# Kernel tuning notes

Measured on AMD Instinct MI355X. Metric: run time of the kernel, lower is better.

## Reference

```python
import jax, jax.numpy as jnp
import numpy as np

N_OUT = 1024

def setup_inputs() -> dict:
    key = jax.random.key(0)
    k1, k2, k3 = jax.random.split(key, 3)
    L, B, n_in = 2048, 16, 1024
    inp = {
        "input": jax.random.normal(k1, (L, B, n_in), dtype=jnp.float32),
        "c_init": jnp.zeros((B, N_OUT), dtype=jnp.float32),
        "weight": jax.random.normal(k2, (n_in, 2 * N_OUT), dtype=jnp.float32) * (1.0 / np.sqrt(n_in)),
        "bias": jax.random.normal(k3, (2 * N_OUT,), dtype=jnp.float32) * 0.1,
    }
    return inp

def reference(input, c_init, weight, bias):
    L, B, n_in = input.shape
    n_out = N_OUT
    # gate pre-activations: [L, B, n_out, 2]
    u_ = jnp.einsum('lbi,io->lbo', input, weight).reshape(L, B, n_out, 2)
    forget_bias = bias.reshape(2, n_out)[1]
    forget = jax.nn.sigmoid(u_[..., 1] + forget_bias)      # [L, B, n_out]
    u0 = u_[..., 0] * (1.0 - forget)                        # [L, B, n_out]

    def step(c_prev, inputs):
        f_t, u_t = inputs
        c_t = c_prev * f_t + u_t
        return c_t, c_t

    c_final, cs = jax.lax.scan(step, c_init, (forget, u0))
    return cs.reshape(L, B, -1), c_final, forget
```

## Files before the change

kernel.cpp:

```cpp
#include <hip/hip_runtime.h>
#include <hip/hip_bf16.h>

#define L_DIM 2048
#define B_DIM 16
#define NIN   1024
#define NOUT  1024
#define M_DIM (L_DIM * B_DIM)
#define N_DIM (2 * NOUT)
#define K_DIM NIN
#define NCOL  (B_DIM * NOUT)
#define NCH   64
#define LC    (L_DIM / NCH)

typedef __bf16 bf16x8 __attribute__((ext_vector_type(8)));
typedef float  f32x4  __attribute__((ext_vector_type(4)));
typedef unsigned short us4 __attribute__((ext_vector_type(4)));

__device__ __forceinline__ unsigned short f2bf(float f) {
    unsigned int u = __float_as_uint(f);
    unsigned int r = (u + 0x7fffu + ((u >> 16) & 1u)) >> 16;
    return (unsigned short)r;
}

__global__ void cvt_input_kernel(const float* __restrict__ in,
                                 unsigned short* __restrict__ out) {
    size_t i = ((size_t)blockIdx.x * 256 + threadIdx.x) * 4;
    float4 v = *(const float4*)(in + i);
    us4 o = { f2bf(v.x), f2bf(v.y), f2bf(v.z), f2bf(v.w) };
    *(us4*)(out + i) = o;
}

__global__ void cvt_weight_kernel(const float* __restrict__ W,
                                  unsigned short* __restrict__ Wt) {
    __shared__ float t[32][33];
    int tx = threadIdx.x, ty = threadIdx.y;
    int i0 = blockIdx.y * 32, n0 = blockIdx.x * 32;
    #pragma unroll
    for (int r = 0; r < 4; ++r)
        t[ty + r * 8][tx] = W[(size_t)(i0 + ty + r * 8) * N_DIM + n0 + tx];
    __syncthreads();
    #pragma unroll
    for (int r = 0; r < 4; ++r)
        Wt[(size_t)(n0 + ty + r * 8) * K_DIM + i0 + tx] = f2bf(t[tx][ty + r * 8]);
}

#define BM 128
#define BN 128
#define BK 32
#define LDAS 40

template<bool PRE_A>
__global__ void gemm_kernel(const float* __restrict__ A32,
                            const unsigned short* __restrict__ Abf,
                            const unsigned short* __restrict__ Wt,
                            const float* __restrict__ bias,
                            float* __restrict__ u0buf,
                            float* __restrict__ fbuf) {
    __shared__ unsigned short As[BM * LDAS];
    __shared__ unsigned short Bs[BN * LDAS];
    __shared__ float sFB[64];

    const int tid = threadIdx.x;
    const int bm = blockIdx.y * BM;
    const int bn = blockIdx.x * BN;
    const int obase = bn >> 1;

    if (tid < 64) sFB[tid] = bias[NOUT + obase + tid];

    const int lane = tid & 63;
    const int wave = tid >> 6;
    const int wr = wave >> 1;
    const int wc = wave & 1;
    const int mrow = lane & 15;
    const int kq = (lane >> 4) * 8;

    f32x4 acc[4][4];
    #pragma unroll
    for (int i = 0; i < 4; ++i)
        #pragma unroll
        for (int j = 0; j < 4; ++j)
            acc[i][j] = (f32x4){0.f, 0.f, 0.f, 0.f};

    for (int k0 = 0; k0 < K_DIM; k0 += BK) {
        if (PRE_A) {
            #pragma unroll
            for (int r = 0; r < 2; ++r) {
                int idx = tid + r * 256;
                int row = idx >> 2;
                int kc  = (idx & 3) << 3;
                *(uint4*)&As[row * LDAS + kc] =
                    *(const uint4*)&Abf[(size_t)(bm + row) * K_DIM + k0 + kc];
            }
        } else {
            #pragma unroll
            for (int r = 0; r < 4; ++r) {
                int idx = tid + r * 256;
                int row = idx >> 3;
                int kc  = (idx & 7) << 2;
                float4 v = *(const float4*)&A32[(size_t)(bm + row) * K_DIM + k0 + kc];
                us4 o = { f2bf(v.x), f2bf(v.y), f2bf(v.z), f2bf(v.w) };
                *(us4*)&As[row * LDAS + kc] = o;
            }
        }
        #pragma unroll
        for (int r = 0; r < 2; ++r) {
            int idx = tid + r * 256;
            int row = idx >> 2;
            int kc  = (idx & 3) << 3;
            *(uint4*)&Bs[row * LDAS + kc] =
                *(const uint4*)&Wt[(size_t)(bn + row) * K_DIM + k0 + kc];
        }
        __syncthreads();

        bf16x8 a[4], b[4];
        #pragma unroll
        for (int mt = 0; mt < 4; ++mt)
            a[mt] = *(const bf16x8*)&As[(wr * 64 + mt * 16 + mrow) * LDAS + kq];
        #pragma unroll
        for (int nt = 0; nt < 4; ++nt)
            b[nt] = *(const bf16x8*)&Bs[(wc * 64 + nt * 16 + mrow) * LDAS + kq];
        #pragma unroll
        for (int mt = 0; mt < 4; ++mt)
            #pragma unroll
            for (int nt = 0; nt < 4; ++nt)
                acc[mt][nt] = __builtin_amdgcn_mfma_f32_16x16x32_bf16(
                    a[mt], b[nt], acc[mt][nt], 0, 0, 0);
        __syncthreads();
    }

    const bool isOdd = (mrow & 1);
    #pragma unroll
    for (int mt = 0; mt < 4; ++mt) {
        #pragma unroll
        for (int nt = 0; nt < 4; ++nt) {
            int gcol = bn + wc * 64 + nt * 16 + mrow;
            int o = gcol >> 1;
            float fb = sFB[o - obase];
            #pragma unroll
            for (int r = 0; r < 4; ++r) {
                float x = acc[mt][nt][r];
                float p = __shfl_xor(x, 1, 64);
                float uo = isOdd ? x : p;
                float f = 1.f / (1.f + __expf(-(uo + fb)));
                int grow = bm + wr * 64 + mt * 16 + (lane >> 4) * 4 + r;
                size_t oi = (size_t)grow * NOUT + o;
                if (isOdd) fbuf[oi]  = f;
                else       u0buf[oi] = x * (1.f - f);
            }
        }
    }
}

__global__ void scan_p1_kernel(const float* __restrict__ fgate,
                               const float* __restrict__ u0,
                               float* __restrict__ Fbuf,
                               float* __restrict__ Ubuf) {
    int j  = blockIdx.x * 256 + threadIdx.x;
    int ch = blockIdx.y;
    size_t base = (size_t)ch * LC * NCOL + j;
    float F = 1.f, U = 0.f;
    #pragma unroll
    for (int l = 0; l < LC; ++l) {
        size_t idx = base + (size_t)l * NCOL;
        float ft = fgate[idx];
        float ut = u0[idx];
        U = fmaf(U, ft, ut);
        F = F * ft;
    }
    Fbuf[(size_t)ch * NCOL + j] = F;
    Ubuf[(size_t)ch * NCOL + j] = U;
}

__global__ void scan_p2_kernel(const float* __restrict__ Fbuf,
                               const float* __restrict__ Ubuf,
                               const float* __restrict__ c_init,
                               float* __restrict__ carry,
                               float* __restrict__ c_final) {
    int j = blockIdx.x * 256 + threadIdx.x;
    float c = c_init[j];
    #pragma unroll
    for (int ch = 0; ch < NCH; ++ch) {
        size_t ci = (size_t)ch * NCOL + j;
        carry[ci] = c;
        c = fmaf(Fbuf[ci], c, Ubuf[ci]);
    }
    c_final[j] = c;
}

__global__ void scan_p3_kernel(const float* __restrict__ fgate,
                               const float* __restrict__ carry,
                               float* __restrict__ cs) {
    int j  = blockIdx.x * 256 + threadIdx.x;
    int ch = blockIdx.y;
    size_t base = (size_t)ch * LC * NCOL + j;
    float c = carry[(size_t)ch * NCOL + j];
    #pragma unroll
    for (int l = 0; l < LC; ++l) {
        size_t idx = base + (size_t)l * NCOL;
        float ft = fgate[idx];
        float ut = cs[idx];
        c = fmaf(c, ft, ut);
        cs[idx] = c;
    }
}

__global__ void scan_kernel(const float* __restrict__ fgate,
                            const float* __restrict__ c_init,
                            float* __restrict__ cs,
                            float* __restrict__ c_final) {
    int j = blockIdx.x * 256 + threadIdx.x;
    float c = c_init[j];
    #pragma unroll 4
    for (int l = 0; l < L_DIM; ++l) {
        size_t idx = (size_t)l * NCOL + j;
        float ft = fgate[idx];
        float u  = cs[idx];
        c = fmaf(c, ft, u);
        cs[idx] = c;
    }
    c_final[j] = c;
}

extern "C" void kernel_launch(void* const* d_in, const int* in_sizes, int n_in,
                              void* d_out, int out_size, void* d_ws, size_t ws_size,
                              hipStream_t stream) {
    const float* input  = (const float*)d_in[0];
    const float* c_init = (const float*)d_in[1];
    const float* weight = (const float*)d_in[2];
    const float* bias   = (const float*)d_in[3];

    float* out_cs = (float*)d_out;
    float* out_cf = out_cs + (size_t)L_DIM * B_DIM * NOUT;
    float* out_fg = out_cf + (size_t)B_DIM * NOUT;

    size_t wt_bytes = (size_t)N_DIM * K_DIM * sizeof(unsigned short);
    size_t wt_pad   = (wt_bytes + 255) & ~(size_t)255;
    size_t a_bytes  = (size_t)M_DIM * K_DIM * sizeof(unsigned short);
    size_t ch_bytes = (size_t)NCH * NCOL * sizeof(float);
    unsigned short* Wt  = (unsigned short*)d_ws;
    unsigned short* Abf = (unsigned short*)((char*)d_ws + wt_pad);
    bool pre_a = (ws_size >= wt_pad + a_bytes);
    size_t scan_off = pre_a ? (wt_pad + a_bytes) : wt_pad;
    float* Fbuf  = (float*)((char*)d_ws + scan_off);
    float* Ubuf  = Fbuf + NCH * NCOL;
    float* carry = Ubuf + NCH * NCOL;
    bool chunked = (ws_size >= scan_off + 3 * ch_bytes);

    cvt_weight_kernel<<<dim3(N_DIM / 32, K_DIM / 32), dim3(32, 8), 0, stream>>>(weight, Wt);

    if (pre_a) {
        int nblk = (M_DIM * K_DIM) / (4 * 256);
        cvt_input_kernel<<<nblk, 256, 0, stream>>>(input, Abf);
    }

    dim3 ggrid(N_DIM / BN, M_DIM / BM);
    if (pre_a)
        gemm_kernel<true ><<<ggrid, 256, 0, stream>>>(input, Abf, Wt, bias, out_cs, out_fg);
    else
        gemm_kernel<false><<<ggrid, 256, 0, stream>>>(input, Abf, Wt, bias, out_cs, out_fg);

    if (chunked) {
        dim3 sgrid(NCOL / 256, NCH);
        scan_p1_kernel<<<sgrid, 256, 0, stream>>>(out_fg, out_cs, Fbuf, Ubuf);
        scan_p2_kernel<<<NCOL / 256, 256, 0, stream>>>(Fbuf, Ubuf, c_init, carry, out_cf);
        scan_p3_kernel<<<sgrid, 256, 0, stream>>>(out_fg, carry, out_cs);
    } else {
        scan_kernel<<<NCOL / 256, 256, 0, stream>>>(out_fg, c_init, out_cs, out_cf);
    }
}
```

Measured before the change: 670.8 us.

## Use direct global-to-LDS loads with swizzled layout in GEMM and vectorize scan passes

The bf16 GEMM path now stages A and B tiles with global_load_lds 16-byte direct loads into an unpadded, XOR-swizzled LDS layout, and remaps workgroup IDs so consecutive blocks spread across output tiles for better cache locality. The chunked scan passes p1 and p3 each process four columns per thread with vector loads and stores, and their grid is shrunk to match. The aim is to cut VGPR round-trips and LDS bank conflicts in tile staging and to raise memory efficiency in the scan. The cost is that correctness depends on the swizzle mapping matching between the load and read sides.

```diff
diff --git a/kernel.cpp b/kernel.cpp
--- a/kernel.cpp
+++ b/kernel.cpp
@@ -22,6 +22,13 @@
     return (unsigned short)r;
 }
 
+__device__ __forceinline__ void gld_lds16(const void* g, void* l) {
+    __builtin_amdgcn_global_load_lds(
+        (const __attribute__((address_space(1))) unsigned int*)g,
+        (__attribute__((address_space(3))) unsigned int*)l,
+        16, 0, 0);
+}
+
 __global__ void cvt_input_kernel(const float* __restrict__ in,
                                  unsigned short* __restrict__ out) {
     size_t i = ((size_t)blockIdx.x * 256 + threadIdx.x) * 4;
@@ -47,22 +54,23 @@
 #define BM 128
 #define BN 128
 #define BK 32
-#define LDAS 40
-
-template<bool PRE_A>
-__global__ void gemm_kernel(const float* __restrict__ A32,
-                            const unsigned short* __restrict__ Abf,
-                            const unsigned short* __restrict__ Wt,
-                            const float* __restrict__ bias,
-                            float* __restrict__ u0buf,
-                            float* __restrict__ fbuf) {
-    __shared__ unsigned short As[BM * LDAS];
-    __shared__ unsigned short Bs[BN * LDAS];
+#define GRID_WG ((M_DIM / BM) * (N_DIM / BN))
+
+__global__ void gemm_lds_kernel(const unsigned short* __restrict__ Abf,
+                                const unsigned short* __restrict__ Wt,
+                                const float* __restrict__ bias,
+                                float* __restrict__ u0buf,
+                                float* __restrict__ fbuf) {
+    __shared__ unsigned short As[BM * BK];
+    __shared__ unsigned short Bs[BN * BK];
     __shared__ float sFB[64];
 
     const int tid = threadIdx.x;
-    const int bm = blockIdx.y * BM;
-    const int bn = blockIdx.x * BN;
+
+    int id = blockIdx.x;
+    int sw = (id & 7) * (GRID_WG / 8) + (id >> 3);
+    const int bm = (sw >> 4) * BM;
+    const int bn = (sw & 15) * BN;
     const int obase = bn >> 1;
 
     if (tid < 64) sFB[tid] = bias[NOUT + obase + tid];
@@ -72,7 +80,19 @@
     const int wr = wave >> 1;
     const int wc = wave & 1;
     const int mrow = lane & 15;
-    const int kq = (lane >> 4) * 8;
+    const int q    = lane >> 4;
+
+    const int srow = lane >> 2;
+    const int logq = (lane & 3) ^ ((lane >> 3) & 3);
+    const int c0 = wave * 2, c1 = c0 + 1;
+    const unsigned short* aS0 = Abf + (size_t)(bm + c0 * 16 + srow) * K_DIM + logq * 8;
+    const unsigned short* aS1 = Abf + (size_t)(bm + c1 * 16 + srow) * K_DIM + logq * 8;
+    const unsigned short* bS0 = Wt  + (size_t)(bn + c0 * 16 + srow) * K_DIM + logq * 8;
+    const unsigned short* bS1 = Wt  + (size_t)(bn + c1 * 16 + srow) * K_DIM + logq * 8;
+    unsigned short* aL0 = &As[c0 * 512];
+    unsigned short* aL1 = &As[c1 * 512];
+    unsigned short* bL0 = &Bs[c0 * 512];
+    unsigned short* bL1 = &Bs[c1 * 512];
 
     f32x4 acc[4][4];
     #pragma unroll
@@ -81,44 +101,22 @@
         for (int j = 0; j < 4; ++j)
             acc[i][j] = (f32x4){0.f, 0.f, 0.f, 0.f};
 
+    const int pq = q ^ ((mrow >> 1) & 3);
+
     for (int k0 = 0; k0 < K_DIM; k0 += BK) {
-        if (PRE_A) {
-            #pragma unroll
-            for (int r = 0; r < 2; ++r) {
-                int idx = tid + r * 256;
-                int row = idx >> 2;
-                int kc  = (idx & 3) << 3;
-                *(uint4*)&As[row * LDAS + kc] =
-                    *(const uint4*)&Abf[(size_t)(bm + row) * K_DIM + k0 + kc];
-            }
-        } else {
-            #pragma unroll
-            for (int r = 0; r < 4; ++r) {
-                int idx = tid + r * 256;
-                int row = idx >> 3;
-                int kc  = (idx & 7) << 2;
-                float4 v = *(const float4*)&A32[(size_t)(bm + row) * K_DIM + k0 + kc];
-                us4 o = { f2bf(v.x), f2bf(v.y), f2bf(v.z), f2bf(v.w) };
-                *(us4*)&As[row * LDAS + kc] = o;
-            }
-        }
-        #pragma unroll
-        for (int r = 0; r < 2; ++r) {
-            int idx = tid + r * 256;
-            int row = idx >> 2;
-            int kc  = (idx & 3) << 3;
-            *(uint4*)&Bs[row * LDAS + kc] =
-                *(const uint4*)&Wt[(size_t)(bn + row) * K_DIM + k0 + kc];
-        }
+        gld_lds16(aS0 + k0, aL0);
+        gld_lds16(aS1 + k0, aL1);
+        gld_lds16(bS0 + k0, bL0);
+        gld_lds16(bS1 + k0, bL1);
         __syncthreads();
 
         bf16x8 a[4], b[4];
         #pragma unroll
         for (int mt = 0; mt < 4; ++mt)
-            a[mt] = *(const bf16x8*)&As[(wr * 64 + mt * 16 + mrow) * LDAS + kq];
+            a[mt] = *(const bf16x8*)&As[(wr * 64 + mt * 16 + mrow) * BK + pq * 8];
         #pragma unroll
         for (int nt = 0; nt < 4; ++nt)
-            b[nt] = *(const bf16x8*)&Bs[(wc * 64 + nt * 16 + mrow) * LDAS + kq];
+            b[nt] = *(const bf16x8*)&Bs[(wc * 64 + nt * 16 + mrow) * BK + pq * 8];
         #pragma unroll
         for (int mt = 0; mt < 4; ++mt)
             #pragma unroll
@@ -151,24 +149,119 @@
     }
 }
 
+#define LDAS 40
+__global__ void gemm_f32_kernel(const float* __restrict__ A32,
+                                const unsigned short* __restrict__ Wt,
+                                const float* __restrict__ bias,
+                                float* __restrict__ u0buf,
+                                float* __restrict__ fbuf) {
+    __shared__ unsigned short As[BM * LDAS];
+    __shared__ unsigned short Bs[BN * LDAS];
+    __shared__ float sFB[64];
+
+    const int tid = threadIdx.x;
+    const int bm = blockIdx.y * BM;
+    const int bn = blockIdx.x * BN;
+    const int obase = bn >> 1;
+
+    if (tid < 64) sFB[tid] = bias[NOUT + obase + tid];
+
+    const int lane = tid & 63;
+    const int wave = tid >> 6;
+    const int wr = wave >> 1;
+    const int wc = wave & 1;
+    const int mrow = lane & 15;
+    const int kq = (lane >> 4) * 8;
+
+    f32x4 acc[4][4];
+    #pragma unroll
+    for (int i = 0; i < 4; ++i)
+        #pragma unroll
+        for (int j = 0; j < 4; ++j)
+            acc[i][j] = (f32x4){0.f, 0.f, 0.f, 0.f};
+
+    for (int k0 = 0; k0 < K_DIM; k0 += BK) {
+        #pragma unroll
+        for (int r = 0; r < 4; ++r) {
+            int idx = tid + r * 256;
+            int row = idx >> 3;
+            int kc  = (idx & 7) << 2;
+            float4 v = *(const float4*)&A32[(size_t)(bm + row) * K_DIM + k0 + kc];
+            us4 o = { f2bf(v.x), f2bf(v.y), f2bf(v.z), f2bf(v.w) };
+            *(us4*)&As[row * LDAS + kc] = o;
+        }
+        #pragma unroll
+        for (int r = 0; r < 2; ++r) {
+            int idx = tid + r * 256;
+            int row = idx >> 2;
+            int kc  = (idx & 3) << 3;
+            *(uint4*)&Bs[row * LDAS + kc] =
+                *(const uint4*)&Wt[(size_t)(bn + row) * K_DIM + k0 + kc];
+        }
+        __syncthreads();
+
+        bf16x8 a[4], b[4];
+        #pragma unroll
+        for (int mt = 0; mt < 4; ++mt)
+            a[mt] = *(const bf16x8*)&As[(wr * 64 + mt * 16 + mrow) * LDAS + kq];
+        #pragma unroll
+        for (int nt = 0; nt < 4; ++nt)
+            b[nt] = *(const bf16x8*)&Bs[(wc * 64 + nt * 16 + mrow) * LDAS + kq];
+        #pragma unroll
+        for (int mt = 0; mt < 4; ++mt)
+            #pragma unroll
+            for (int nt = 0; nt < 4; ++nt)
+                acc[mt][nt] = __builtin_amdgcn_mfma_f32_16x16x32_bf16(
+                    a[mt], b[nt], acc[mt][nt], 0, 0, 0);
+        __syncthreads();
+    }
+
+    const bool isOdd = (mrow & 1);
+    #pragma unroll
+    for (int mt = 0; mt < 4; ++mt) {
+        #pragma unroll
+        for (int nt = 0; nt < 4; ++nt) {
+            int gcol = bn + wc * 64 + nt * 16 + mrow;
+            int o = gcol >> 1;
+            float fb = sFB[o - obase];
+            #pragma unroll
+            for (int r = 0; r < 4; ++r) {
+                float x = acc[mt][nt][r];
+                float p = __shfl_xor(x, 1, 64);
+                float uo = isOdd ? x : p;
+                float f = 1.f / (1.f + __expf(-(uo + fb)));
+                int grow = bm + wr * 64 + mt * 16 + (lane >> 4) * 4 + r;
+                size_t oi = (size_t)grow * NOUT + o;
+                if (isOdd) fbuf[oi]  = f;
+                else       u0buf[oi] = x * (1.f - f);
+            }
+        }
+    }
+}
+
 __global__ void scan_p1_kernel(const float* __restrict__ fgate,
                                const float* __restrict__ u0,
                                float* __restrict__ Fbuf,
                                float* __restrict__ Ubuf) {
-    int j  = blockIdx.x * 256 + threadIdx.x;
+    int j4 = blockIdx.x * 256 + threadIdx.x;
     int ch = blockIdx.y;
-    size_t base = (size_t)ch * LC * NCOL + j;
-    float F = 1.f, U = 0.f;
-    #pragma unroll
+    size_t base = (size_t)ch * LC * NCOL + (size_t)j4 * 4;
+    f32x4 F = {1.f, 1.f, 1.f, 1.f};
+    f32x4 U = {0.f, 0.f, 0.f, 0.f};
+    #pragma unroll 8
     for (int l = 0; l < LC; ++l) {
         size_t idx = base + (size_t)l * NCOL;
-        float ft = fgate[idx];
-        float ut = u0[idx];
-        U = fmaf(U, ft, ut);
-        F = F * ft;
-    }
-    Fbuf[(size_t)ch * NCOL + j] = F;
-    Ubuf[(size_t)ch * NCOL + j] = U;
+        f32x4 ft = *(const f32x4*)(fgate + idx);
+        f32x4 ut = *(const f32x4*)(u0 + idx);
+        #pragma unroll
+        for (int c = 0; c < 4; ++c) {
+            U[c] = fmaf(U[c], ft[c], ut[c]);
+            F[c] = F[c] * ft[c];
+        }
+    }
+    size_t ci = (size_t)ch * NCOL + (size_t)j4 * 4;
+    *(f32x4*)(Fbuf + ci) = F;
+    *(f32x4*)(Ubuf + ci) = U;
 }
 
 __global__ void scan_p2_kernel(const float* __restrict__ Fbuf,
@@ -190,17 +283,19 @@
 __global__ void scan_p3_kernel(const float* __restrict__ fgate,
                                const float* __restrict__ carry,
                                float* __restrict__ cs) {
-    int j  = blockIdx.x * 256 + threadIdx.x;
+    int j4 = blockIdx.x * 256 + threadIdx.x;
     int ch = blockIdx.y;
-    size_t base = (size_t)ch * LC * NCOL + j;
-    float c = carry[(size_t)ch * NCOL + j];
-    #pragma unroll
+    size_t base = (size_t)ch * LC * NCOL + (size_t)j4 * 4;
+    f32x4 c = *(const f32x4*)(carry + (size_t)ch * NCOL + (size_t)j4 * 4);
+    #pragma unroll 8
     for (int l = 0; l < LC; ++l) {
         size_t idx = base + (size_t)l * NCOL;
-        float ft = fgate[idx];
-        float ut = cs[idx];
-        c = fmaf(c, ft, ut);
-        cs[idx] = c;
+        f32x4 ft = *(const f32x4*)(fgate + idx);
+        f32x4 ut = *(const f32x4*)(cs + idx);
+        #pragma unroll
+        for (int cc = 0; cc < 4; ++cc)
+            c[cc] = fmaf(c[cc], ft[cc], ut[cc]);
+        *(f32x4*)(cs + idx) = c;
     }
 }
 
@@ -253,14 +348,15 @@
         cvt_input_kernel<<<nblk, 256, 0, stream>>>(input, Abf);
     }
 
-    dim3 ggrid(N_DIM / BN, M_DIM / BM);
-    if (pre_a)
-        gemm_kernel<true ><<<ggrid, 256, 0, stream>>>(input, Abf, Wt, bias, out_cs, out_fg);
-    else
-        gemm_kernel<false><<<ggrid, 256, 0, stream>>>(input, Abf, Wt, bias, out_cs, out_fg);
+    if (pre_a) {
+        gemm_lds_kernel<<<GRID_WG, 256, 0, stream>>>(Abf, Wt, bias, out_cs, out_fg);
+    } else {
+        dim3 ggrid(N_DIM / BN, M_DIM / BM);
+        gemm_f32_kernel<<<ggrid, 256, 0, stream>>>(input, Wt, bias, out_cs, out_fg);
+    }
 
     if (chunked) {
-        dim3 sgrid(NCOL / 256, NCH);
+        dim3 sgrid(NCOL / 1024, NCH);
         scan_p1_kernel<<<sgrid, 256, 0, stream>>>(out_fg, out_cs, Fbuf, Ubuf);
         scan_p2_kernel<<<NCOL / 256, 256, 0, stream>>>(Fbuf, Ubuf, c_init, carry, out_cf);
         scan_p3_kernel<<<sgrid, 256, 0, stream>>>(out_fg, carry, out_cs);
```

Measured after the change: 650.3 us. 3.1% less time.
